# Kernel optimization log

Hardware: AMD Instinct MI355X
Metric: run time of the kernel (lower is better)

## Reference

```python
import jax, jax.numpy as jnp
import numpy as np

N_POINTS = 8192
D_FEAT = 256
WEIGHT = 1.0  # self.weight
EPS = 1e-12


def _pairwise_dist(x):
    # Euclidean pairwise distances, [N, N]
    sq = jnp.sum(x * x, axis=-1)
    d2 = sq[:, None] + sq[None, :] - 2.0 * (x @ x.T)
    d2 = jnp.maximum(d2, 0.0)
    return jnp.sqrt(d2 + EPS)


def _mst_edge_weights(dist):
    # Prim's algorithm, vectorized O(N^2). The MST edge lengths are exactly
    # the death times of the H0 (dim-0) persistence diagram of the
    # Vietoris-Rips filtration (all births = 0). jit-compatible via lax.scan.
    n = dist.shape[0]
    big = jnp.asarray(1e30, dist.dtype)
    in_tree0 = jnp.zeros((n,), dtype=bool).at[0].set(True)
    mindist0 = dist[0]

    def step(carry, _):
        in_tree, mindist = carry
        masked = jnp.where(in_tree, big, mindist)
        j = jnp.argmin(masked)
        w = masked[j]                      # weight of MST edge added this step
        in_tree = in_tree.at[j].set(True)
        mindist = jnp.minimum(mindist, dist[j])
        return (in_tree, mindist), w

    _, weights = jax.lax.scan(step, (in_tree0, mindist0), None, length=n - 1)
    return weights  # [N-1] H0 death times


def _persistent_entropy(lifetimes):
    # PersistentEntropy.compute: p_i = l_i / sum(l); E = -sum p_i log p_i
    total = jnp.sum(lifetimes)
    p = lifetimes / (total + EPS)
    return -jnp.sum(p * jnp.log(p + EPS))


def setup_inputs() -> dict:
    key = jax.random.key(0)
    representations = jax.random.normal(key, (N_POINTS, D_FEAT), dtype=jnp.float32)
    return {"representations": representations}


def reference(representations):
    # PersistentHomology.compute_from_distance: VR filtration over the point
    # cloud; H0 diagram computed exactly via MST (single-linkage). Higher
    # dims (dim=1) are not produced, so the `if dim < len(diagrams)` guard
    # skips them, matching GPU PH implementations that emit H0 only.
    dist = _pairwise_dist(representations)
    deaths = _mst_edge_weights(dist)
    entropy = _persistent_entropy(deaths)
    loss = -entropy  # target_entropy is None -> maximize entropy
    return WEIGHT * loss
```

## Files before the change

kernel.cpp:

```cpp
#include <hip/hip_runtime.h>
#include <hip/hip_bf16.h>
#include <hip/hip_fp16.h>

#define NP 8192
#define DF 256
#define PH1 4
#define PH2 9
#define NC 512
#define CAND_K 48
#define NBINS 2048
#define ALLR 13

typedef unsigned long long u64;
typedef unsigned int u32;
typedef unsigned short u16;
using bf16x8 = __attribute__((ext_vector_type(8))) short;
using f32x4  = __attribute__((ext_vector_type(4))) float;
using u16x8  = __attribute__((ext_vector_type(8))) u16;

__device__ __forceinline__ u16 f2bf(float f) {
  __hip_bfloat16 h = __float2bfloat16(f);
  return __builtin_bit_cast(u16, h);
}
__device__ __forceinline__ u16 f2h_bits(float f) {
  _Float16 h = (_Float16)f;
  return __builtin_bit_cast(u16, h);
}
__device__ __forceinline__ u64 mkkey(u32 vbits, int i, int j) {
  int lo = i < j ? i : j;
  int hi = i ^ j ^ lo;
  return ((u64)vbits << 26) | ((u64)lo << 13) | (u64)hi;
}


__global__ void init_kernel(int* comp, u64* compmin, int* edgeCnt, int* nComps, int* fbCnt) {
  int i = blockIdx.x * 256 + threadIdx.x;
  if (i < NP) { comp[i] = i; compmin[i] = ~0ull; }
  if (blockIdx.x == 0 && threadIdx.x < 16) fbCnt[threadIdx.x] = 0;
  if (i == 0) { *edgeCnt = 0; *nComps = NP; }
}


__global__ __launch_bounds__(64) void sq_kernel(const float* __restrict__ X, float* __restrict__ sq) {
  int i = blockIdx.x;
  float4 v = ((const float4*)(X + (size_t)i * DF))[threadIdx.x];
  float s = v.x * v.x + v.y * v.y + v.z * v.z + v.w * v.w;
#pragma unroll
  for (int off = 32; off >= 1; off >>= 1) s += __shfl_down(s, off);
  if (threadIdx.x == 0) sq[i] = s;
}


__global__ __launch_bounds__(256) void cvt_kernel(const float* __restrict__ X, u16* __restrict__ Xb) {
  int idx = (blockIdx.x * 256 + threadIdx.x) * 8;
  float4 a = ((const float4*)(X + idx))[0];
  float4 b = ((const float4*)(X + idx))[1];
  u16x8 o;
  o[0] = f2bf(a.x); o[1] = f2bf(a.y); o[2] = f2bf(a.z); o[3] = f2bf(a.w);
  o[4] = f2bf(b.x); o[5] = f2bf(b.y); o[6] = f2bf(b.z); o[7] = f2bf(b.w);
  *(u16x8*)(Xb + idx) = o;
}


template <bool PRE>
__global__ __launch_bounds__(256) void build_dist_kernel(
    const float* __restrict__ X, const u16* __restrict__ Xb,
    const float* __restrict__ sq, _Float16* __restrict__ d2) {
  __shared__ __align__(16) u16 smem[128 * 144];
  u16* At = smem;
  u16* Bt = smem + 128 * 40;
  const int t = threadIdx.x;
  const int m0 = blockIdx.y * 128, n0 = blockIdx.x * 128;
  const int wid = t >> 6, lane = t & 63;
  const int wm = wid >> 1, wn = wid & 1;
  const int lrow = lane & 15, lk = lane >> 4;
  f32x4 acc[4][4] = {};

  const int srow = t >> 1, shalf = t & 1;
  for (int k0 = 0; k0 < DF; k0 += 32) {
    u16x8 av0, av1, bv0, bv1;
    if (PRE) {
      const u16* pa = Xb + (size_t)(m0 + srow) * DF + k0 + shalf * 16;
      av0 = *(const u16x8*)pa; av1 = *(const u16x8*)(pa + 8);
      const u16* pb = Xb + (size_t)(n0 + srow) * DF + k0 + shalf * 16;
      bv0 = *(const u16x8*)pb; bv1 = *(const u16x8*)(pb + 8);
    } else {
      const float4* pa = (const float4*)(X + (size_t)(m0 + srow) * DF + k0 + shalf * 16);
      float4 a0 = pa[0], a1 = pa[1], a2 = pa[2], a3 = pa[3];
      av0[0]=f2bf(a0.x); av0[1]=f2bf(a0.y); av0[2]=f2bf(a0.z); av0[3]=f2bf(a0.w);
      av0[4]=f2bf(a1.x); av0[5]=f2bf(a1.y); av0[6]=f2bf(a1.z); av0[7]=f2bf(a1.w);
      av1[0]=f2bf(a2.x); av1[1]=f2bf(a2.y); av1[2]=f2bf(a2.z); av1[3]=f2bf(a2.w);
      av1[4]=f2bf(a3.x); av1[5]=f2bf(a3.y); av1[6]=f2bf(a3.z); av1[7]=f2bf(a3.w);
      const float4* pb = (const float4*)(X + (size_t)(n0 + srow) * DF + k0 + shalf * 16);
      float4 b0 = pb[0], b1 = pb[1], b2 = pb[2], b3 = pb[3];
      bv0[0]=f2bf(b0.x); bv0[1]=f2bf(b0.y); bv0[2]=f2bf(b0.z); bv0[3]=f2bf(b0.w);
      bv0[4]=f2bf(b1.x); bv0[5]=f2bf(b1.y); bv0[6]=f2bf(b1.z); bv0[7]=f2bf(b1.w);
      bv1[0]=f2bf(b2.x); bv1[1]=f2bf(b2.y); bv1[2]=f2bf(b2.z); bv1[3]=f2bf(b2.w);
      bv1[4]=f2bf(b3.x); bv1[5]=f2bf(b3.y); bv1[6]=f2bf(b3.z); bv1[7]=f2bf(b3.w);
    }
    __syncthreads();
    *(u16x8*)&At[srow * 40 + shalf * 16] = av0;
    *(u16x8*)&At[srow * 40 + shalf * 16 + 8] = av1;
    *(u16x8*)&Bt[srow * 40 + shalf * 16] = bv0;
    *(u16x8*)&Bt[srow * 40 + shalf * 16 + 8] = bv1;
    __syncthreads();
    bf16x8 af[4], bfr[4];
#pragma unroll
    for (int fm = 0; fm < 4; ++fm)
      af[fm] = *(const bf16x8*)&At[(wm * 64 + fm * 16 + lrow) * 40 + lk * 8];
#pragma unroll
    for (int fn = 0; fn < 4; ++fn)
      bfr[fn] = *(const bf16x8*)&Bt[(wn * 64 + fn * 16 + lrow) * 40 + lk * 8];
#pragma unroll
    for (int fm = 0; fm < 4; ++fm)
#pragma unroll
      for (int fn = 0; fn < 4; ++fn)
        acc[fm][fn] = __builtin_amdgcn_mfma_f32_16x16x32_bf16(af[fm], bfr[fn], acc[fm][fn], 0, 0, 0);
  }
  __syncthreads();

  float sqj[4];
#pragma unroll
  for (int fn = 0; fn < 4; ++fn) sqj[fn] = sq[n0 + wn * 64 + fn * 16 + lrow];
#pragma unroll
  for (int fm = 0; fm < 4; ++fm) {
#pragma unroll
    for (int r = 0; r < 4; ++r) {
      int row = wm * 64 + fm * 16 + lk * 4 + r;
      int i = m0 + row;
      float si = sq[i];
#pragma unroll
      for (int fn = 0; fn < 4; ++fn) {
        int col = wn * 64 + fn * 16 + lrow;
        float dd = si + sqj[fn] - 2.0f * acc[fm][fn][r];
        dd = fmaxf(dd, 0.0f);
        if (i == n0 + col) dd = INFINITY;
        smem[row * 144 + col] = f2h_bits(dd);
      }
    }
  }
  __syncthreads();
#pragma unroll
  for (int k = 0; k < 8; ++k) {
    int flat = k * 256 + t;
    int row = flat >> 4, cb = (flat & 15) * 8;
    *(u16x8*)&d2[(size_t)(m0 + row) * NP + n0 + cb] = *(const u16x8*)&smem[row * 144 + cb];
  }
}


__global__ __launch_bounds__(256) void topk_kernel(const _Float16* __restrict__ d2,
                                                   u64* __restrict__ candT,
                                                   u32* __restrict__ candCnt) {
  __shared__ u16 rowbuf[NP];
  __shared__ u32 hist[NBINS];
  __shared__ u32 scanw[4];
  __shared__ int swred[4];
  __shared__ int sB;
  __shared__ u32 sCnt;
  const int i = blockIdx.x;
  const int t = threadIdx.x;
  const u16* row = (const u16*)(d2 + (size_t)i * NP);
  for (int b = t; b < NBINS; b += 256) hist[b] = 0;
  if (t == 0) sCnt = 0;
  __syncthreads();
  for (int base = t * 8; base < NP; base += 2048) {
    u16x8 v = *(const u16x8*)(row + base);
    *(u16x8*)&rowbuf[base] = v;
#pragma unroll
    for (int q = 0; q < 8; ++q) atomicAdd(&hist[v[q] >> 5], 1u);
  }
  __syncthreads();
  u32 loc[8]; u32 s = 0;
#pragma unroll
  for (int q = 0; q < 8; ++q) { loc[q] = hist[t * 8 + q]; s += loc[q]; }
  u32 pre = s;
  for (int off = 1; off < 64; off <<= 1) {
    u32 o = __shfl_up(pre, off);
    if ((t & 63) >= off) pre += o;
  }
  if ((t & 63) == 63) scanw[t >> 6] = pre;
  __syncthreads();
  u32 wbase = 0;
  for (int w = 0; w < (t >> 6); ++w) wbase += scanw[w];
  u32 c = wbase + pre - s;
  int lb = -1;
#pragma unroll
  for (int q = 0; q < 8; ++q) {
    c += loc[q];
    if (c >= 1 && c <= CAND_K) lb = t * 8 + q;
  }
#pragma unroll
  for (int off = 32; off >= 1; off >>= 1) {
    int o = __shfl_down(lb, off);
    lb = lb > o ? lb : o;
  }
  if ((t & 63) == 0) swred[t >> 6] = lb;
  __syncthreads();
  if (t == 0) {
    int m = swred[0];
#pragma unroll
    for (int w = 1; w < 4; ++w) m = m > swred[w] ? m : swred[w];
    sB = m;
  }
  __syncthreads();
  const int B = sB;
  if (B >= 0) {
    for (int base = t * 8; base < NP; base += 2048) {
#pragma unroll
      for (int q = 0; q < 8; ++q) {
        u16 v = rowbuf[base + q];
        if ((int)(v >> 5) <= B) {
          u32 pos = atomicAdd(&sCnt, 1u);
          if (pos < CAND_K) candT[(size_t)pos * NP + i] = mkkey(v, i, base + q);
        }
      }
    }
  }
  __syncthreads();
  if (t == 0) {
    u32 n = sCnt;
    candCnt[i] = (n == 0 || n > CAND_K) ? 0x80000000u : n;
  }
}


__global__ __launch_bounds__(256) void cand_min_kernel(
    const u64* __restrict__ candT, const u32* __restrict__ candCnt,
    const int* __restrict__ comp, u64* __restrict__ compmin,
    const int* __restrict__ nComps, int* __restrict__ fbList,
    int* __restrict__ fbCnt, int r) {
  if (*nComps == 1) return;
  const int i = blockIdx.x * 256 + threadIdx.x;
  const int ci = comp[i];
  u32 cc = candCnt[i];
  int n = (int)(cc & 0x7fffffffu);
  u64 best = ~0ull;
  for (int k = 0; k < n; ++k) {
    u64 key = candT[(size_t)k * NP + i];
    int lo = (int)((key >> 13) & 0x1FFF);
    int hi = (int)(key & 0x1FFF);
    int j = (lo == i) ? hi : lo;
    if (comp[j] != ci && key < best) best = key;
  }
  if (best != ~0ull && !(cc & 0x80000000u)) {
    atomicMin(&compmin[ci], best);
  } else {
    int p = atomicAdd(&fbCnt[r], 1);
    fbList[p] = i;
  }
}


__global__ __launch_bounds__(256) void fb_kernel(
    const _Float16* __restrict__ d2, const int* __restrict__ comp,
    u64* __restrict__ compmin, const int* __restrict__ fbList,
    const int* __restrict__ fbCnt, int r, const int* __restrict__ nComps) {
  if (*nComps == 1) return;
  __shared__ u64 sred[4];
  const int t = threadIdx.x;
  const int n = fbCnt[r];
  for (int idx = blockIdx.x; idx < n; idx += gridDim.x) {
    const int i = fbList[idx];
    const int ci = comp[i];
    const u16* row = (const u16*)(d2 + (size_t)i * NP);
    u64 best = ~0ull;
    for (int base = t * 8; base < NP; base += 2048) {
      u16x8 v = *(const u16x8*)(row + base);
      int4 c0 = *(const int4*)(comp + base);
      int4 c1 = *(const int4*)(comp + base + 4);
      int cs[8] = {c0.x, c0.y, c0.z, c0.w, c1.x, c1.y, c1.z, c1.w};
#pragma unroll
      for (int q = 0; q < 8; ++q) {
        if (cs[q] != ci) {
          u64 k = mkkey(v[q], i, base + q);
          best = k < best ? k : best;
        }
      }
    }
#pragma unroll
    for (int off = 32; off >= 1; off >>= 1) {
      u64 o = __shfl_down(best, off);
      best = best < o ? best : o;
    }
    if ((t & 63) == 0) sred[t >> 6] = best;
    __syncthreads();
    if (t == 0) {
      best = sred[0];
#pragma unroll
      for (int w = 1; w < 4; ++w) best = best < sred[w] ? best : sred[w];
      if (best != ~0ull) atomicMin(&compmin[ci], best);
    }
    __syncthreads();
  }
}


__global__ void select_kernel(const float* __restrict__ X, const float* __restrict__ sq,
                              const int* __restrict__ comp, const u64* __restrict__ compmin,
                              int* __restrict__ parent, float* __restrict__ edgeW,
                              int* __restrict__ edgeCnt, const int* __restrict__ nComps) {
  int c = blockIdx.x * blockDim.x + threadIdx.x;
  if (c >= NP) return;
  if (*nComps == 1) { parent[c] = c; return; }
  u64 m = compmin[c];
  if (m == ~0ull) { parent[c] = c; return; }
  int a = (int)((m >> 13) & 0x1FFF);
  int b = (int)(m & 0x1FFF);
  int j = (comp[a] == c) ? b : a;
  int d = comp[j];
  bool mutual = false;
  u64 md = compmin[d];
  if (md != ~0ull) {
    int a2 = (int)((md >> 13) & 0x1FFF);
    int b2 = (int)(md & 0x1FFF);
    int j2 = (comp[a2] == d) ? b2 : a2;
    mutual = (comp[j2] == c);
  }
  if (mutual && c > d) { parent[c] = d; return; }
  parent[c] = mutual ? c : d;
  const float4* pa = (const float4*)(X + (size_t)a * DF);
  const float4* pb = (const float4*)(X + (size_t)b * DF);
  float dot = 0.f;
#pragma unroll 8
  for (int k = 0; k < DF / 4; ++k) {
    float4 va = pa[k], vb = pb[k];
    dot += va.x * vb.x + va.y * vb.y + va.z * vb.z + va.w * vb.w;
  }
  float dd = sq[a] + sq[b] - 2.f * dot;
  float w = sqrtf(fmaxf(dd, 0.f) + 1e-12f);
  int idx = atomicAdd(edgeCnt, 1);
  if (idx < NP) edgeW[idx] = w;
}


template <bool DENSE>
__global__ __launch_bounds__(1024) void jump_relabel_kernel(
    const int* __restrict__ parent, int* __restrict__ comp,
    u64* __restrict__ compmin, int* __restrict__ nComps,
    u16* __restrict__ dcomp, int* __restrict__ comp2, int* __restrict__ parent2,
    u64* __restrict__ compmin2, int* __restrict__ ncDense) {
  if (*nComps == 1) return;
  __shared__ int sp[NP];
  __shared__ u16 did[NP];
  __shared__ int swsum[16];
  __shared__ int scnt;
  __shared__ int sch;
  const int t = threadIdx.x;
  const int lane = t & 63, wv = t >> 6;
  for (int c = t; c < NP; c += 1024) { sp[c] = parent[c]; did[c] = 0; }
  if (t == 0) { scnt = 0; sch = 0; }
  __syncthreads();
  for (int it = 0; it < 13; ++it) {
    int ch = 0;
    for (int c = t; c < NP; c += 1024) {
      int p = sp[c];
      int pp = sp[p];
      if (p != pp) { sp[c] = pp; ch = 1; }
    }
    if (ch) sch = 1;
    __syncthreads();
    if (!sch) break;
    __syncthreads();
    if (t == 0) sch = 0;
    __syncthreads();
  }
  for (int i = t; i < NP; i += 1024) {
    int nc = sp[comp[i]];
    comp[i] = nc;
    did[nc] = 1;
  }
  __syncthreads();
  if constexpr (!DENSE) {
    int part = 0;
    for (int c = t; c < NP; c += 1024) part += did[c];
#pragma unroll
    for (int off = 32; off >= 1; off >>= 1) part += __shfl_down(part, off);
    if (lane == 0) atomicAdd(&scnt, part);
    for (int c = t; c < NP; c += 1024) compmin[c] = ~0ull;
    __syncthreads();
    if (t == 0) *nComps = scnt;
  } else {
    int f[8]; int s = 0;
#pragma unroll
    for (int q = 0; q < 8; ++q) { f[q] = did[t * 8 + q]; s += f[q]; }
    int incl = s;
    for (int off = 1; off < 64; off <<= 1) {
      int o = __shfl_up(incl, off);
      if (lane >= off) incl += o;
    }
    if (lane == 63) swsum[wv] = incl;
    __syncthreads();
    int wbase = 0;
    for (int w = 0; w < wv; ++w) wbase += swsum[w];
    int e = wbase + incl - s;
#pragma unroll
    for (int q = 0; q < 8; ++q) {
      if (f[q]) { did[t * 8 + q] = (u16)e; ++e; }
    }
    __syncthreads();
    for (int i = t; i < NP; i += 1024) dcomp[i] = did[comp[i]];
    if (t < NC) { comp2[t] = t; parent2[t] = t; compmin2[t] = ~0ull; }
    if (t == 0) {
      int total = 0;
#pragma unroll
      for (int w = 0; w < 16; ++w) total += swsum[w];
      *nComps = total;
      *ncDense = total;
    }
  }
}


__global__ __launch_bounds__(256) void minit_kernel(u64* __restrict__ M) {
  int idx = (blockIdx.x * 256 + threadIdx.x) * 4;
#pragma unroll
  for (int q = 0; q < 4; ++q) M[idx + q] = ~0ull;
}


__global__ __launch_bounds__(256) void contract_kernel(
    const _Float16* __restrict__ d2, const u16* __restrict__ dcomp,
    u64* __restrict__ M) {
  __shared__ u32 table[NC];
  const int i = blockIdx.x;
  const int t = threadIdx.x;
  for (int b = t; b < NC; b += 256) table[b] = ~0u;
  __syncthreads();
  const int ci = dcomp[i];
  const u16* row = (const u16*)(d2 + (size_t)i * NP);
  for (int base = t * 8; base < NP; base += 2048) {
    u16x8 v = *(const u16x8*)(row + base);
    u16x8 cj = *(const u16x8*)(dcomp + base);
#pragma unroll
    for (int q = 0; q < 8; ++q) {
      if (cj[q] != ci) {
        u32 k32 = ((u32)v[q] << 13) | (u32)(base + q);
        atomicMin(&table[cj[q]], k32);
      }
    }
  }
  __syncthreads();
  for (int b = t; b < NC; b += 256) {
    u32 k32 = table[b];
    if (k32 != ~0u) {
      u64 key = mkkey(k32 >> 13, i, (int)(k32 & 0x1FFF));
      u64* addr = &M[(size_t)ci * NC + b];
      if (key < *addr) atomicMin(addr, key);
    }
  }
}


__global__ __launch_bounds__(64) void rmin2_kernel(const u64* __restrict__ M,
                                                   const int* __restrict__ comp2,
                                                   u64* __restrict__ compmin2,
                                                   const int* __restrict__ nComps) {
  if (*nComps == 1) return;
  const int a = blockIdx.x;
  const int t = threadIdx.x;
  const int ca = comp2[a];
  u64 best = ~0ull;
  for (int b = t; b < NC; b += 64) {
    u64 k = M[(size_t)a * NC + b];
    if (k != ~0ull && comp2[b] != ca && k < best) best = k;
  }
#pragma unroll
  for (int off = 32; off >= 1; off >>= 1) {
    u64 o = __shfl_down(best, off);
    best = best < o ? best : o;
  }
  if (t == 0 && best != ~0ull) atomicMin(&compmin2[ca], best);
}


__global__ void select2_kernel(const float* __restrict__ X, const float* __restrict__ sq,
                               const u16* __restrict__ dcomp, const int* __restrict__ comp2,
                               const u64* __restrict__ compmin2, int* __restrict__ parent2,
                               float* __restrict__ edgeW, int* __restrict__ edgeCnt,
                               const int* __restrict__ nComps) {
  int c = blockIdx.x * blockDim.x + threadIdx.x;
  if (c >= NC) return;
  if (*nComps == 1) { parent2[c] = c; return; }
  u64 m = compmin2[c];
  if (m == ~0ull) { parent2[c] = c; return; }
  int a = (int)((m >> 13) & 0x1FFF);
  int b = (int)(m & 0x1FFF);
  int j = (comp2[dcomp[a]] == c) ? b : a;
  int d = comp2[dcomp[j]];
  bool mutual = false;
  u64 md = compmin2[d];
  if (md != ~0ull) {
    int a2 = (int)((md >> 13) & 0x1FFF);
    int b2 = (int)(md & 0x1FFF);
    int j2 = (comp2[dcomp[a2]] == d) ? b2 : a2;
    mutual = (comp2[dcomp[j2]] == c);
  }
  if (mutual && c > d) { parent2[c] = d; return; }
  parent2[c] = mutual ? c : d;
  const float4* pa = (const float4*)(X + (size_t)a * DF);
  const float4* pb = (const float4*)(X + (size_t)b * DF);
  float dot = 0.f;
#pragma unroll 8
  for (int k = 0; k < DF / 4; ++k) {
    float4 va = pa[k], vb = pb[k];
    dot += va.x * vb.x + va.y * vb.y + va.z * vb.z + va.w * vb.w;
  }
  float dd = sq[a] + sq[b] - 2.f * dot;
  float w = sqrtf(fmaxf(dd, 0.f) + 1e-12f);
  int idx = atomicAdd(edgeCnt, 1);
  if (idx < NP) edgeW[idx] = w;
}


__global__ __launch_bounds__(NC) void jump2_kernel(const int* __restrict__ parent2,
                                                   int* __restrict__ comp2,
                                                   u64* __restrict__ compmin2,
                                                   int* __restrict__ nComps,
                                                   const int* __restrict__ ncDense) {
  if (*nComps == 1) return;
  __shared__ int sp[NC];
  __shared__ u16 fl[NC];
  __shared__ int scnt;
  const int t = threadIdx.x;
  sp[t] = parent2[t];
  fl[t] = 0;
  if (t == 0) scnt = 0;
  __syncthreads();
#pragma unroll
  for (int it = 0; it < 9; ++it) {
    sp[t] = sp[sp[t]];
    __syncthreads();
  }
  int nd = *ncDense;
  int nc2 = sp[comp2[t]];
  comp2[t] = nc2;
  if (t < nd) fl[nc2] = 1;
  __syncthreads();
  int part = fl[t];
#pragma unroll
  for (int off = 32; off >= 1; off >>= 1) part += __shfl_down(part, off);
  if ((t & 63) == 0) atomicAdd(&scnt, part);
  compmin2[t] = ~0ull;
  __syncthreads();
  if (t == 0) *nComps = scnt;
}


__global__ __launch_bounds__(1024) void entropy_kernel(const float* __restrict__ edgeW,
                                                       const int* __restrict__ edgeCnt,
                                                       float* __restrict__ out) {
  __shared__ float sred[16];
  __shared__ float stot;
  int ne = *edgeCnt;
  if (ne > NP) ne = NP;
  float s = 0.f;
  for (int k = threadIdx.x; k < ne; k += 1024) s += edgeW[k];
#pragma unroll
  for (int off = 32; off >= 1; off >>= 1) s += __shfl_down(s, off);
  int lane = threadIdx.x & 63, wv = threadIdx.x >> 6;
  if (lane == 0) sred[wv] = s;
  __syncthreads();
  if (threadIdx.x == 0) {
    float tt = 0.f;
#pragma unroll
    for (int w = 0; w < 16; ++w) tt += sred[w];
    stot = tt;
  }
  __syncthreads();
  float total = stot;
  float acc = 0.f;
  for (int k = threadIdx.x; k < ne; k += 1024) {
    float p = edgeW[k] / (total + 1e-12f);
    acc += p * logf(p + 1e-12f);
  }
#pragma unroll
  for (int off = 32; off >= 1; off >>= 1) acc += __shfl_down(acc, off);
  if (lane == 0) sred[wv] = acc;
  __syncthreads();
  if (threadIdx.x == 0) {
    float tt = 0.f;
#pragma unroll
    for (int w = 0; w < 16; ++w) tt += sred[w];
    out[0] = tt;
  }
}


extern "C" void kernel_launch(void* const* d_in, const int* in_sizes, int n_in,
                              void* d_out, int out_size, void* d_ws, size_t ws_size,
                              hipStream_t stream) {
  const float* X = (const float*)d_in[0];
  float* out = (float*)d_out;
  char* ws = (char*)d_ws;

  const size_t nn = (size_t)NP * NP;
  size_t off = (nn * 2 + 255) & ~(size_t)255;
  _Float16* d2 = (_Float16*)ws;
  float* sq = (float*)(ws + off);      off += (size_t)NP * 4;
  int* comp = (int*)(ws + off);        off += (size_t)NP * 4;
  u64* compmin = (u64*)(ws + off);     off += (size_t)NP * 8;
  int* parent = (int*)(ws + off);      off += (size_t)NP * 4;
  float* edgeW = (float*)(ws + off);   off += (size_t)NP * 4;
  u32* candCnt = (u32*)(ws + off);     off += (size_t)NP * 4;
  int* fbList = (int*)(ws + off);      off += (size_t)NP * 4;
  u16* dcomp = (u16*)(ws + off);       off += (size_t)NP * 2;
  int* comp2 = (int*)(ws + off);       off += (size_t)NC * 4;
  int* parent2 = (int*)(ws + off);     off += (size_t)NC * 4;
  u64* compmin2 = (u64*)(ws + off);    off += (size_t)NC * 8;
  int* edgeCnt = (int*)(ws + off);     off += 64;
  int* nComps = (int*)(ws + off);      off += 64;
  int* ncDense = (int*)(ws + off);     off += 64;
  int* fbCnt = (int*)(ws + off);       off += 64;
  off = (off + 255) & ~(size_t)255;
  u16* Xb = (u16*)(ws + off);
  u64* candT = (u64*)(ws + off);
  u64* M = (u64*)(ws + off);
  const bool PRE = (ws_size >= off + (size_t)NP * DF * 2);
  const bool useM = (ws_size >= off + (size_t)NC * NC * 8);

  init_kernel<<<NP / 256, 256, 0, stream>>>(comp, compmin, edgeCnt, nComps, fbCnt);
  sq_kernel<<<NP, 64, 0, stream>>>(X, sq);
  if (PRE) {
    cvt_kernel<<<NP * DF / (256 * 8), 256, 0, stream>>>(X, Xb);
    build_dist_kernel<true><<<dim3(NP / 128, NP / 128), 256, 0, stream>>>(X, Xb, sq, d2);
  } else {
    build_dist_kernel<false><<<dim3(NP / 128, NP / 128), 256, 0, stream>>>(X, Xb, sq, d2);
  }
  topk_kernel<<<NP, 256, 0, stream>>>(d2, candT, candCnt);

  const int p1 = useM ? PH1 : ALLR;
  for (int r = 0; r < p1; ++r) {
    cand_min_kernel<<<NP / 256, 256, 0, stream>>>(candT, candCnt, comp, compmin, nComps,
                                                  fbList, fbCnt, r);
    fb_kernel<<<128, 256, 0, stream>>>(d2, comp, compmin, fbList, fbCnt, r, nComps);
    select_kernel<<<NP / 256, 256, 0, stream>>>(X, sq, comp, compmin, parent, edgeW,
                                                edgeCnt, nComps);
    if (useM && r == p1 - 1) {
      jump_relabel_kernel<true><<<1, 1024, 0, stream>>>(parent, comp, compmin, nComps,
                                                        dcomp, comp2, parent2, compmin2, ncDense);
    } else {
      jump_relabel_kernel<false><<<1, 1024, 0, stream>>>(parent, comp, compmin, nComps,
                                                         dcomp, comp2, parent2, compmin2, ncDense);
    }
  }

  if (useM) {
    minit_kernel<<<NC * NC / (256 * 4), 256, 0, stream>>>(M);
    contract_kernel<<<NP, 256, 0, stream>>>(d2, dcomp, M);
    for (int r = 0; r < PH2; ++r) {
      rmin2_kernel<<<NC, 64, 0, stream>>>(M, comp2, compmin2, nComps);
      select2_kernel<<<NC / 256, 256, 0, stream>>>(X, sq, dcomp, comp2, compmin2, parent2,
                                                   edgeW, edgeCnt, nComps);
      jump2_kernel<<<1, NC, 0, stream>>>(parent2, comp2, compmin2, nComps, ncDense);
    }
  }

  entropy_kernel<<<1, 1024, 0, stream>>>(edgeW, edgeCnt, out);
}
```

Baseline: 459.1 us.

## Store candidates row-major, reduce per wavefront, fuse phase-2 select with jump

Candidate keys are now stored row-major with a padded stride of 64 per point, and cand_min assigns one wavefront per point, with each lane handling one candidate and a shuffle reduction producing the minimum. This replaces the serial per-thread loop over a transposed array with parallel loads. The phase-2 select and pointer-jump kernels are merged into a single-block kernel that keeps parent links in shared memory, removing one launch per round and the parent2 buffer. The fallback condition no longer checks the overflow flag directly, because an overflowed count of zero leaves best unset and still sends the point to the fallback path.

```diff
diff --git a/kernel.cpp b/kernel.cpp
--- a/kernel.cpp
+++ b/kernel.cpp
@@ -8,6 +8,7 @@
 #define PH2 9
 #define NC 512
 #define CAND_K 48
+#define CAND_PAD 64
 #define NBINS 2048
 #define ALLR 13
 
@@ -150,7 +151,7 @@
 
 
 __global__ __launch_bounds__(256) void topk_kernel(const _Float16* __restrict__ d2,
-                                                   u64* __restrict__ candT,
+                                                   u64* __restrict__ candR,
                                                    u32* __restrict__ candCnt) {
   __shared__ u16 rowbuf[NP];
   __shared__ u32 hist[NBINS];
@@ -212,7 +213,7 @@
         u16 v = rowbuf[base + q];
         if ((int)(v >> 5) <= B) {
           u32 pos = atomicAdd(&sCnt, 1u);
-          if (pos < CAND_K) candT[(size_t)pos * NP + i] = mkkey(v, i, base + q);
+          if (pos < CAND_K) candR[(size_t)i * CAND_PAD + pos] = mkkey(v, i, base + q);
         }
       }
     }
@@ -226,28 +227,37 @@
 
 
 __global__ __launch_bounds__(256) void cand_min_kernel(
-    const u64* __restrict__ candT, const u32* __restrict__ candCnt,
+    const u64* __restrict__ candR, const u32* __restrict__ candCnt,
     const int* __restrict__ comp, u64* __restrict__ compmin,
     const int* __restrict__ nComps, int* __restrict__ fbList,
     int* __restrict__ fbCnt, int r) {
   if (*nComps == 1) return;
-  const int i = blockIdx.x * 256 + threadIdx.x;
+  const int t = threadIdx.x;
+  const int lane = t & 63;
+  const int i = blockIdx.x * 4 + (t >> 6);
   const int ci = comp[i];
-  u32 cc = candCnt[i];
-  int n = (int)(cc & 0x7fffffffu);
+  const u32 cc = candCnt[i];
+  const int n = (int)(cc & 0x7fffffffu);
   u64 best = ~0ull;
-  for (int k = 0; k < n; ++k) {
-    u64 key = candT[(size_t)k * NP + i];
+  if (lane < n) {
+    u64 key = candR[(size_t)i * CAND_PAD + lane];
     int lo = (int)((key >> 13) & 0x1FFF);
     int hi = (int)(key & 0x1FFF);
     int j = (lo == i) ? hi : lo;
-    if (comp[j] != ci && key < best) best = key;
-  }
-  if (best != ~0ull && !(cc & 0x80000000u)) {
-    atomicMin(&compmin[ci], best);
-  } else {
-    int p = atomicAdd(&fbCnt[r], 1);
-    fbList[p] = i;
+    if (comp[j] != ci) best = key;
+  }
+#pragma unroll
+  for (int off = 32; off >= 1; off >>= 1) {
+    u64 o = __shfl_xor(best, off);
+    best = best < o ? best : o;
+  }
+  if (lane == 0) {
+    if (best != ~0ull) {
+      atomicMin(&compmin[ci], best);
+    } else {
+      int p = atomicAdd(&fbCnt[r], 1);
+      fbList[p] = i;
+    }
   }
 }
 
@@ -338,7 +348,7 @@
 __global__ __launch_bounds__(1024) void jump_relabel_kernel(
     const int* __restrict__ parent, int* __restrict__ comp,
     u64* __restrict__ compmin, int* __restrict__ nComps,
-    u16* __restrict__ dcomp, int* __restrict__ comp2, int* __restrict__ parent2,
+    u16* __restrict__ dcomp, int* __restrict__ comp2,
     u64* __restrict__ compmin2, int* __restrict__ ncDense) {
   if (*nComps == 1) return;
   __shared__ int sp[NP];
@@ -400,7 +410,7 @@
     }
     __syncthreads();
     for (int i = t; i < NP; i += 1024) dcomp[i] = did[comp[i]];
-    if (t < NC) { comp2[t] = t; parent2[t] = t; compmin2[t] = ~0ull; }
+    if (t < NC) { comp2[t] = t; compmin2[t] = ~0ull; }
     if (t == 0) {
       int total = 0;
 #pragma unroll
@@ -474,58 +484,58 @@
 }
 
 
-__global__ void select2_kernel(const float* __restrict__ X, const float* __restrict__ sq,
-                               const u16* __restrict__ dcomp, const int* __restrict__ comp2,
-                               const u64* __restrict__ compmin2, int* __restrict__ parent2,
-                               float* __restrict__ edgeW, int* __restrict__ edgeCnt,
-                               const int* __restrict__ nComps) {
-  int c = blockIdx.x * blockDim.x + threadIdx.x;
-  if (c >= NC) return;
-  if (*nComps == 1) { parent2[c] = c; return; }
-  u64 m = compmin2[c];
-  if (m == ~0ull) { parent2[c] = c; return; }
-  int a = (int)((m >> 13) & 0x1FFF);
-  int b = (int)(m & 0x1FFF);
-  int j = (comp2[dcomp[a]] == c) ? b : a;
-  int d = comp2[dcomp[j]];
-  bool mutual = false;
-  u64 md = compmin2[d];
-  if (md != ~0ull) {
-    int a2 = (int)((md >> 13) & 0x1FFF);
-    int b2 = (int)(md & 0x1FFF);
-    int j2 = (comp2[dcomp[a2]] == d) ? b2 : a2;
-    mutual = (comp2[dcomp[j2]] == c);
-  }
-  if (mutual && c > d) { parent2[c] = d; return; }
-  parent2[c] = mutual ? c : d;
-  const float4* pa = (const float4*)(X + (size_t)a * DF);
-  const float4* pb = (const float4*)(X + (size_t)b * DF);
-  float dot = 0.f;
-#pragma unroll 8
-  for (int k = 0; k < DF / 4; ++k) {
-    float4 va = pa[k], vb = pb[k];
-    dot += va.x * vb.x + va.y * vb.y + va.z * vb.z + va.w * vb.w;
-  }
-  float dd = sq[a] + sq[b] - 2.f * dot;
-  float w = sqrtf(fmaxf(dd, 0.f) + 1e-12f);
-  int idx = atomicAdd(edgeCnt, 1);
-  if (idx < NP) edgeW[idx] = w;
-}
-
-
-__global__ __launch_bounds__(NC) void jump2_kernel(const int* __restrict__ parent2,
-                                                   int* __restrict__ comp2,
-                                                   u64* __restrict__ compmin2,
-                                                   int* __restrict__ nComps,
-                                                   const int* __restrict__ ncDense) {
+__global__ __launch_bounds__(NC) void sel_jump2_kernel(
+    const float* __restrict__ X, const float* __restrict__ sq,
+    const u16* __restrict__ dcomp, int* __restrict__ comp2,
+    u64* __restrict__ compmin2, float* __restrict__ edgeW,
+    int* __restrict__ edgeCnt, int* __restrict__ nComps,
+    const int* __restrict__ ncDense) {
   if (*nComps == 1) return;
   __shared__ int sp[NC];
   __shared__ u16 fl[NC];
   __shared__ int scnt;
   const int t = threadIdx.x;
-  sp[t] = parent2[t];
+  int par = t;
+  bool doEdge = false;
+  int ea = 0, eb = 0;
+  u64 m = compmin2[t];
+  if (m != ~0ull) {
+    int a = (int)((m >> 13) & 0x1FFF);
+    int b = (int)(m & 0x1FFF);
+    int j = (comp2[dcomp[a]] == t) ? b : a;
+    int d = comp2[dcomp[j]];
+    bool mutual = false;
+    u64 md = compmin2[d];
+    if (md != ~0ull) {
+      int a2 = (int)((md >> 13) & 0x1FFF);
+      int b2 = (int)(md & 0x1FFF);
+      int j2 = (comp2[dcomp[a2]] == d) ? b2 : a2;
+      mutual = (comp2[dcomp[j2]] == t);
+    }
+    if (mutual && t > d) {
+      par = d;
+    } else {
+      par = mutual ? t : d;
+      doEdge = true; ea = a; eb = b;
+    }
+  }
+  sp[t] = par;
   fl[t] = 0;
   if (t == 0) scnt = 0;
+  if (doEdge) {
+    const float4* pa = (const float4*)(X + (size_t)ea * DF);
+    const float4* pb = (const float4*)(X + (size_t)eb * DF);
+    float dot = 0.f;
+#pragma unroll 8
+    for (int k = 0; k < DF / 4; ++k) {
+      float4 va = pa[k], vb = pb[k];
+      dot += va.x * vb.x + va.y * vb.y + va.z * vb.z + va.w * vb.w;
+    }
+    float dd = sq[ea] + sq[eb] - 2.f * dot;
+    float w = sqrtf(fmaxf(dd, 0.f) + 1e-12f);
+    int idx = atomicAdd(edgeCnt, 1);
+    if (idx < NP) edgeW[idx] = w;
+  }
   __syncthreads();
 #pragma unroll
   for (int it = 0; it < 9; ++it) {
@@ -606,7 +616,6 @@
   int* fbList = (int*)(ws + off);      off += (size_t)NP * 4;
   u16* dcomp = (u16*)(ws + off);       off += (size_t)NP * 2;
   int* comp2 = (int*)(ws + off);       off += (size_t)NC * 4;
-  int* parent2 = (int*)(ws + off);     off += (size_t)NC * 4;
   u64* compmin2 = (u64*)(ws + off);    off += (size_t)NC * 8;
   int* edgeCnt = (int*)(ws + off);     off += 64;
   int* nComps = (int*)(ws + off);      off += 64;
@@ -614,9 +623,10 @@
   int* fbCnt = (int*)(ws + off);       off += 64;
   off = (off + 255) & ~(size_t)255;
   u16* Xb = (u16*)(ws + off);
-  u64* candT = (u64*)(ws + off);
+  u64* candR = (u64*)(ws + off);
   u64* M = (u64*)(ws + off);
-  const bool PRE = (ws_size >= off + (size_t)NP * DF * 2);
+  const size_t regionR = (size_t)NP * CAND_PAD * 8;
+  const bool PRE = (ws_size >= off + regionR);
   const bool useM = (ws_size >= off + (size_t)NC * NC * 8);
 
   init_kernel<<<NP / 256, 256, 0, stream>>>(comp, compmin, edgeCnt, nComps, fbCnt);
@@ -627,21 +637,21 @@
   } else {
     build_dist_kernel<false><<<dim3(NP / 128, NP / 128), 256, 0, stream>>>(X, Xb, sq, d2);
   }
-  topk_kernel<<<NP, 256, 0, stream>>>(d2, candT, candCnt);
+  topk_kernel<<<NP, 256, 0, stream>>>(d2, candR, candCnt);
 
   const int p1 = useM ? PH1 : ALLR;
   for (int r = 0; r < p1; ++r) {
-    cand_min_kernel<<<NP / 256, 256, 0, stream>>>(candT, candCnt, comp, compmin, nComps,
-                                                  fbList, fbCnt, r);
+    cand_min_kernel<<<NP / 4, 256, 0, stream>>>(candR, candCnt, comp, compmin, nComps,
+                                                fbList, fbCnt, r);
     fb_kernel<<<128, 256, 0, stream>>>(d2, comp, compmin, fbList, fbCnt, r, nComps);
     select_kernel<<<NP / 256, 256, 0, stream>>>(X, sq, comp, compmin, parent, edgeW,
                                                 edgeCnt, nComps);
     if (useM && r == p1 - 1) {
       jump_relabel_kernel<true><<<1, 1024, 0, stream>>>(parent, comp, compmin, nComps,
-                                                        dcomp, comp2, parent2, compmin2, ncDense);
+                                                        dcomp, comp2, compmin2, ncDense);
     } else {
       jump_relabel_kernel<false><<<1, 1024, 0, stream>>>(parent, comp, compmin, nComps,
-                                                         dcomp, comp2, parent2, compmin2, ncDense);
+                                                         dcomp, comp2, compmin2, ncDense);
     }
   }
 
@@ -650,9 +660,8 @@
     contract_kernel<<<NP, 256, 0, stream>>>(d2, dcomp, M);
     for (int r = 0; r < PH2; ++r) {
       rmin2_kernel<<<NC, 64, 0, stream>>>(M, comp2, compmin2, nComps);
-      select2_kernel<<<NC / 256, 256, 0, stream>>>(X, sq, dcomp, comp2, compmin2, parent2,
-                                                   edgeW, edgeCnt, nComps);
-      jump2_kernel<<<1, NC, 0, stream>>>(parent2, comp2, compmin2, nComps, ncDense);
+      sel_jump2_kernel<<<1, NC, 0, stream>>>(X, sq, dcomp, comp2, compmin2,
+                                             edgeW, edgeCnt, nComps, ncDense);
     }
   }
 
```

Measured after the change: 408.6 us. 11.0% less time.
